# Performance work log

Hardware: AMD Instinct MI355X
Metric: run time of the kernel (lower is better)

Reference implementation:

```python
import jax, jax.numpy as jnp
import numpy as np

N_NODES = 100000
N_EDGES = 1600000
IN_F = 128
HID = 128
OUT_F = 40


def _gcn_conv(x, W, b, src, dst):
    # PyG GCNConv: h = x @ W; out[dst] += norm * h[src]; out += b
    n = x.shape[0]
    h = x @ W  # [N, out_channels]
    deg = jnp.zeros((n,), h.dtype).at[dst].add(jnp.ones((dst.shape[0],), h.dtype))
    dinv = jnp.where(deg > 0, jax.lax.rsqrt(deg), 0.0)  # deg^{-1/2}
    norm = dinv[src] * dinv[dst]  # [E+N]
    msg = h[src] * norm[:, None]  # [E+N, out_channels] gather
    out = jnp.zeros_like(h).at[dst].add(msg)  # scatter-add at targets
    if b is not None:
        out = out + b
    return out


def setup_inputs() -> dict:
    key = jax.random.key(0)
    k_x, k_e, k1, k2, k3, kb1, kb2 = jax.random.split(key, 7)
    x = jax.random.normal(k_x, (N_NODES, IN_F), dtype=jnp.float32)
    edge_index = jax.random.randint(k_e, (2, N_EDGES), 0, N_NODES, dtype=jnp.int64)
    s_in = 1.0 / np.sqrt(IN_F)
    s_h = 1.0 / np.sqrt(HID)
    W_in = jax.random.normal(k1, (IN_F, HID), dtype=jnp.float32) * s_in
    b_in = jnp.zeros((HID,), dtype=jnp.float32)
    W_mid = jax.random.normal(k2, (HID, HID), dtype=jnp.float32) * s_h
    b_mid = jnp.zeros((HID,), dtype=jnp.float32)
    W_out = jax.random.normal(k3, (HID, OUT_F), dtype=jnp.float32) * s_h
    return {"x": x, "edge_index": edge_index, "W_in": W_in, "b_in": b_in,
            "W_mid": W_mid, "b_mid": b_mid, "W_out": W_out}


def reference(x, edge_index, W_in, b_in, W_mid, b_mid, W_out):
    n = x.shape[0]
    loops = jnp.arange(n, dtype=edge_index.dtype)
    src = jnp.concatenate([edge_index[0], loops])  # add self-loops
    dst = jnp.concatenate([edge_index[1], loops])
    h = jax.nn.relu(_gcn_conv(x, W_in, b_in, src, dst))
    h = jax.nn.relu(_gcn_conv(h, W_mid, b_mid, src, dst))
    h = _gcn_conv(h, W_out, None, src, dst)  # out_conv: bias=False
    return jax.nn.log_softmax(h, axis=1)
```

## Files before the change

### kernel.cpp

```cpp
#include <hip/hip_runtime.h>
#include <math.h>

#define N_NODES 100000
#define N_EDGES 1600000
#define NBUCK 391
#define BSTRIDE 4608

typedef __attribute__((ext_vector_type(8))) _Float16 h8v;
typedef __attribute__((ext_vector_type(4))) float f32x4;
typedef __attribute__((ext_vector_type(2))) int i32x2;

#define GEMM_GRID 625
#define NTILES 3125


__global__ void k_prep(const int* __restrict__ srcv, const int* __restrict__ dstv,
                       int* __restrict__ bcnt, unsigned int* __restrict__ ebuf,
                       const float* __restrict__ x, const float* __restrict__ W1,
                       const float* __restrict__ W2, const float* __restrict__ W3,
                       _Float16* __restrict__ Wt,
                       _Float16* __restrict__ bufA, _Float16* __restrict__ bufB,
                       _Float16* __restrict__ zbuf) {
    const int tid = threadIdx.x;
    const int bid = blockIdx.x;

    if (bid < 625) {
        const int lane = tid & 63;
        const int wi = tid >> 6;
        const int nb = wi * 32;
        const int nn = lane & 15;
        const int quad = lane >> 4;
        const int kq = quad * 8;

        h8v bh[4][2], bl[4][2];
#pragma unroll
        for (int c = 0; c < 4; c++)
#pragma unroll
            for (int t = 0; t < 2; t++) {
#pragma unroll
                for (int j = 0; j < 8; j++) {
                    float w = W1[(c * 32 + kq + j) * 128 + nb + t * 16 + nn];
                    _Float16 hi = (_Float16)w;
                    bh[c][t][j] = hi;
                    bl[c][t][j] = (_Float16)(w - (float)hi);
                }
            }

        for (int rt = bid; rt < NTILES; rt += GEMM_GRID) {
            const int r0 = rt * 32;
            f32x4 acc[2][2] = {};
#pragma unroll
            for (int c = 0; c < 4; c++) {
                h8v a[2];
#pragma unroll
                for (int m = 0; m < 2; m++) {
                    const float* p = x + (size_t)(r0 + m * 16 + nn) * 128 + c * 32 + kq;
                    float4 p0 = *(const float4*)p;
                    float4 p1 = *(const float4*)(p + 4);
                    h8v av = {(_Float16)p0.x, (_Float16)p0.y, (_Float16)p0.z, (_Float16)p0.w,
                              (_Float16)p1.x, (_Float16)p1.y, (_Float16)p1.z, (_Float16)p1.w};
                    a[m] = av;
                }
#pragma unroll
                for (int m = 0; m < 2; m++)
#pragma unroll
                    for (int t = 0; t < 2; t++) {
                        acc[m][t] = __builtin_amdgcn_mfma_f32_16x16x32_f16(a[m], bh[c][t], acc[m][t], 0, 0, 0);
                        acc[m][t] = __builtin_amdgcn_mfma_f32_16x16x32_f16(a[m], bl[c][t], acc[m][t], 0, 0, 0);
                    }
            }
#pragma unroll
            for (int m = 0; m < 2; m++)
#pragma unroll
                for (int reg = 0; reg < 4; reg++) {
                    int r = r0 + m * 16 + quad * 4 + reg;
#pragma unroll
                    for (int t = 0; t < 2; t++)
                        bufA[(size_t)r * 128 + nb + t * 16 + nn] = (_Float16)acc[m][t][reg];
                }
        }
        return;
    }

    if (bid >= 1016) {
        if (bid == 1104) {
            if (tid < 128) {
                bufA[(size_t)N_NODES * 128 + tid] = (_Float16)0.f;
                bufB[(size_t)N_NODES * 128 + tid] = (_Float16)0.f;
            }
            if (tid < 64)  zbuf[(size_t)N_NODES * 64 + tid] = (_Float16)0.f;
            return;
        }
        int idx = (bid - 1016) * 256 + tid;
        if (idx >= 176 * 128) return;
        int n = idx / 128, k = idx % 128;
        _Float16 *ph, *pl;
        float v;
        if (n < 128) {
            v = W2[k * 128 + n];
            ph = Wt + 2 * 128 * 128; pl = Wt + 3 * 128 * 128;
        } else {
            int nloc = n - 128;
            v = (nloc < 40) ? W3[k * 40 + nloc] : 0.f;
            ph = Wt + 4 * 128 * 128; pl = Wt + 4 * 128 * 128 + 48 * 128;
            n = nloc;
        }
        _Float16 hi = (_Float16)v;
        _Float16 lo = (_Float16)(v - (float)hi);
        ph[n * 128 + k] = hi;
        pl[n * 128 + k] = lo;
        return;
    }

    __shared__ int hist[NBUCK];
    __shared__ int cur[NBUCK];
    for (int t = tid; t < NBUCK; t += 256) hist[t] = 0;
    __syncthreads();
    const int base = (bid - 625) * 4096;
#pragma unroll
    for (int i = 0; i < 16; i++) {
        int e = base + i * 256 + tid;
        if (e < N_EDGES) atomicAdd(&hist[dstv[e] >> 8], 1);
    }
    __syncthreads();
    for (int t = tid; t < NBUCK; t += 256)
        if (hist[t]) cur[t] = t * BSTRIDE + atomicAdd(&bcnt[t], hist[t]);
    __syncthreads();
#pragma unroll
    for (int i = 0; i < 16; i++) {
        int e = base + i * 256 + tid;
        if (e < N_EDGES) {
            int d = dstv[e];
            int p = atomicAdd(&cur[d >> 8], 1);
            ebuf[p] = ((unsigned int)srcv[e] << 8) | (unsigned int)(d & 255);
        }
    }
}

__launch_bounds__(256)
__global__ void k_bucket(const unsigned int* __restrict__ ebuf, const int* __restrict__ bcnt,
                         i32x2* __restrict__ rowse, float* __restrict__ dinv,
                         int* __restrict__ colidx) {
    __shared__ int cnt[256];
    __shared__ int s[256];
    __shared__ int cur[256];
    const int tid = threadIdx.x;
    const int b = blockIdx.x;
    if (b == 0 && tid == 0) dinv[N_NODES] = 0.f;
    const int e0 = b * BSTRIDE;
    const int e1 = e0 + bcnt[b];
    cnt[tid] = 0;
    __syncthreads();
    for (int e = e0 + tid; e < e1; e += 256) atomicAdd(&cnt[ebuf[e] & 255u], 1);
    __syncthreads();
    int v = cnt[tid];
    int x = v;
    s[tid] = x;
    __syncthreads();
    for (int d = 1; d < 256; d <<= 1) {
        int t = (tid >= d) ? s[tid - d] : 0;
        __syncthreads();
        x += t;
        s[tid] = x;
        __syncthreads();
    }
    int start = e0 + x - v;
    int node = b * 256 + tid;
    if (node < N_NODES) {
        i32x2 se;
        se.x = start;
        se.y = start + v;
        rowse[node] = se;
        dinv[node] = rsqrtf((float)(v + 1));
    }
    cur[tid] = start;
    __syncthreads();
    for (int e = e0 + tid; e < e1; e += 256) {
        unsigned int sd = ebuf[e];
        int pos = atomicAdd(&cur[sd & 255u], 1);
        colidx[pos] = (int)(sd >> 8);
    }
}


__launch_bounds__(256)
__global__ void k_fused128(const _Float16* __restrict__ hp, const i32x2* __restrict__ rowse,
                           const int* __restrict__ colidx, const float* __restrict__ bias,
                           const float* __restrict__ dinv,
                           const _Float16* __restrict__ Wthi, const _Float16* __restrict__ Wtlo,
                           _Float16* __restrict__ out) {
    __shared__ __align__(16) _Float16 As[16 * 128];
    const int lane = threadIdx.x & 63;
    const int wi = threadIdx.x >> 6;
    const int nn = lane & 15;
    const int quad = lane >> 4;
    const int r0 = blockIdx.x * 16;

    {
        const int rl = wi * 4 + quad;
        const int r = r0 + rl;
        const i32x2 se = rowse[r];
        const int deg = se.y - se.x;
        int m = deg;
        m = max(m, __shfl_xor(m, 16));
        m = max(m, __shfl_xor(m, 32));
        const _Float16* hpc = hp + nn * 8;
        float accf[8] = {};
        for (int it = 0; it < m; it += 4) {
            int i0 = se.x + it;
            int s0 = colidx[i0];
            int s1 = colidx[i0 + 1];
            int s2 = colidx[i0 + 2];
            int s3 = colidx[i0 + 3];
            s0 = (it < deg) ? s0 : N_NODES;
            s1 = (it + 1 < deg) ? s1 : N_NODES;
            s2 = (it + 2 < deg) ? s2 : N_NODES;
            s3 = (it + 3 < deg) ? s3 : N_NODES;
            float d0 = dinv[s0];
            float d1 = dinv[s1];
            float d2 = dinv[s2];
            float d3 = dinv[s3];
            h8v v0 = *(const h8v*)(hpc + (size_t)s0 * 128);
            h8v v1 = *(const h8v*)(hpc + (size_t)s1 * 128);
            h8v v2 = *(const h8v*)(hpc + (size_t)s2 * 128);
            h8v v3 = *(const h8v*)(hpc + (size_t)s3 * 128);
#pragma unroll
            for (int j = 0; j < 8; j++) {
                accf[j] = fmaf(d0, (float)v0[j], accf[j]);
                accf[j] = fmaf(d1, (float)v1[j], accf[j]);
                accf[j] = fmaf(d2, (float)v2[j], accf[j]);
                accf[j] = fmaf(d3, (float)v3[j], accf[j]);
            }
        }
        h8v sv = *(const h8v*)(hpc + (size_t)r * 128);
        float dv = rsqrtf((float)(deg + 1));
        const float* bp = bias + nn * 8;
        float4 b0 = *(const float4*)bp;
        float4 b1 = *(const float4*)(bp + 4);
        float bb[8] = {b0.x, b0.y, b0.z, b0.w, b1.x, b1.y, b1.z, b1.w};
        h8v o;
#pragma unroll
        for (int j = 0; j < 8; j++) {
            float sx = accf[j] + dv * (float)sv[j];
            o[j] = (_Float16)fmaxf(fmaf(dv, sx, bb[j]), 0.f);
        }
        *(h8v*)(As + rl * 128 + ((nn ^ rl) * 8)) = o;
    }
    __syncthreads();

    const int nb = wi * 32;
    const int kq = quad * 8;
    f32x4 acc2[2] = {};
#pragma unroll
    for (int c = 0; c < 4; c++) {
        int ch = (c * 4 + quad) ^ nn;
        h8v a = *(const h8v*)(As + nn * 128 + ch * 8);
#pragma unroll
        for (int t = 0; t < 2; t++) {
            int off = (nb + t * 16 + nn) * 128 + c * 32 + kq;
            h8v bhv = *(const h8v*)(Wthi + off);
            h8v blv = *(const h8v*)(Wtlo + off);
            acc2[t] = __builtin_amdgcn_mfma_f32_16x16x32_f16(a, bhv, acc2[t], 0, 0, 0);
            acc2[t] = __builtin_amdgcn_mfma_f32_16x16x32_f16(a, blv, acc2[t], 0, 0, 0);
        }
    }
#pragma unroll
    for (int reg = 0; reg < 4; reg++) {
        int r = r0 + quad * 4 + reg;
#pragma unroll
        for (int t = 0; t < 2; t++)
            out[(size_t)r * 128 + nb + t * 16 + nn] = (_Float16)acc2[t][reg];
    }
}

__launch_bounds__(256)
__global__ void k_fused40(const _Float16* __restrict__ hp, const i32x2* __restrict__ rowse,
                          const int* __restrict__ colidx, const float* __restrict__ bias,
                          const float* __restrict__ dinv,
                          const _Float16* __restrict__ Wthi, const _Float16* __restrict__ Wtlo,
                          _Float16* __restrict__ out) {
    __shared__ __align__(16) _Float16 As[16 * 128];
    const int lane = threadIdx.x & 63;
    const int wi = threadIdx.x >> 6;
    const int nn = lane & 15;
    const int quad = lane >> 4;
    const int r0 = blockIdx.x * 16;

    {
        const int rl = wi * 4 + quad;
        const int r = r0 + rl;
        const i32x2 se = rowse[r];
        const int deg = se.y - se.x;
        int m = deg;
        m = max(m, __shfl_xor(m, 16));
        m = max(m, __shfl_xor(m, 32));
        const _Float16* hpc = hp + nn * 8;
        float accf[8] = {};
        for (int it = 0; it < m; it += 4) {
            int i0 = se.x + it;
            int s0 = colidx[i0];
            int s1 = colidx[i0 + 1];
            int s2 = colidx[i0 + 2];
            int s3 = colidx[i0 + 3];
            s0 = (it < deg) ? s0 : N_NODES;
            s1 = (it + 1 < deg) ? s1 : N_NODES;
            s2 = (it + 2 < deg) ? s2 : N_NODES;
            s3 = (it + 3 < deg) ? s3 : N_NODES;
            float d0 = dinv[s0];
            float d1 = dinv[s1];
            float d2 = dinv[s2];
            float d3 = dinv[s3];
            h8v v0 = *(const h8v*)(hpc + (size_t)s0 * 128);
            h8v v1 = *(const h8v*)(hpc + (size_t)s1 * 128);
            h8v v2 = *(const h8v*)(hpc + (size_t)s2 * 128);
            h8v v3 = *(const h8v*)(hpc + (size_t)s3 * 128);
#pragma unroll
            for (int j = 0; j < 8; j++) {
                accf[j] = fmaf(d0, (float)v0[j], accf[j]);
                accf[j] = fmaf(d1, (float)v1[j], accf[j]);
                accf[j] = fmaf(d2, (float)v2[j], accf[j]);
                accf[j] = fmaf(d3, (float)v3[j], accf[j]);
            }
        }
        h8v sv = *(const h8v*)(hpc + (size_t)r * 128);
        float dv = rsqrtf((float)(deg + 1));
        const float* bp = bias + nn * 8;
        float4 b0 = *(const float4*)bp;
        float4 b1 = *(const float4*)(bp + 4);
        float bb[8] = {b0.x, b0.y, b0.z, b0.w, b1.x, b1.y, b1.z, b1.w};
        h8v o;
#pragma unroll
        for (int j = 0; j < 8; j++) {
            float sx = accf[j] + dv * (float)sv[j];
            o[j] = (_Float16)fmaxf(fmaf(dv, sx, bb[j]), 0.f);
        }
        *(h8v*)(As + rl * 128 + ((nn ^ rl) * 8)) = o;
    }
    __syncthreads();

    if (wi < 3) {
        const int kq = quad * 8;
        f32x4 acc2 = {};
#pragma unroll
        for (int c = 0; c < 4; c++) {
            int ch = (c * 4 + quad) ^ nn;
            h8v a = *(const h8v*)(As + nn * 128 + ch * 8);
            int off = (wi * 16 + nn) * 128 + c * 32 + kq;
            h8v bhv = *(const h8v*)(Wthi + off);
            h8v blv = *(const h8v*)(Wtlo + off);
            acc2 = __builtin_amdgcn_mfma_f32_16x16x32_f16(a, bhv, acc2, 0, 0, 0);
            acc2 = __builtin_amdgcn_mfma_f32_16x16x32_f16(a, blv, acc2, 0, 0, 0);
        }
#pragma unroll
        for (int reg = 0; reg < 4; reg++) {
            int r = r0 + quad * 4 + reg;
            out[(size_t)r * 64 + wi * 16 + nn] = (_Float16)acc2[reg];
        }
    }
}


__launch_bounds__(256)
__global__ void k_agg_out(const _Float16* __restrict__ hp, const i32x2* __restrict__ rowse,
                          const int* __restrict__ colidx, const float* __restrict__ dinv,
                          float* __restrict__ out) {
    const int lane = threadIdx.x & 63;
    const int wid = (blockIdx.x * blockDim.x + threadIdx.x) >> 6;
    const int rs = lane >> 3;
    const int cp = lane & 7;
    const int r = wid * 8 + rs;

    const i32x2 se = rowse[r];
    const int deg = se.y - se.x;
    int m = deg;
    m = max(m, __shfl_xor(m, 8));
    m = max(m, __shfl_xor(m, 16));
    m = max(m, __shfl_xor(m, 32));

    const _Float16* hpc = hp + cp * 8;
    float accf[8] = {};
    for (int it = 0; it < m; it += 4) {
        int i0 = se.x + it;
        int s0 = colidx[i0];
        int s1 = colidx[i0 + 1];
        int s2 = colidx[i0 + 2];
        int s3 = colidx[i0 + 3];
        s0 = (it < deg) ? s0 : N_NODES;
        s1 = (it + 1 < deg) ? s1 : N_NODES;
        s2 = (it + 2 < deg) ? s2 : N_NODES;
        s3 = (it + 3 < deg) ? s3 : N_NODES;
        float d0 = dinv[s0];
        float d1 = dinv[s1];
        float d2 = dinv[s2];
        float d3 = dinv[s3];
        h8v v0 = *(const h8v*)(hpc + (size_t)s0 * 64);
        h8v v1 = *(const h8v*)(hpc + (size_t)s1 * 64);
        h8v v2 = *(const h8v*)(hpc + (size_t)s2 * 64);
        h8v v3 = *(const h8v*)(hpc + (size_t)s3 * 64);
#pragma unroll
        for (int j = 0; j < 8; j++) {
            accf[j] = fmaf(d0, (float)v0[j], accf[j]);
            accf[j] = fmaf(d1, (float)v1[j], accf[j]);
            accf[j] = fmaf(d2, (float)v2[j], accf[j]);
            accf[j] = fmaf(d3, (float)v3[j], accf[j]);
        }
    }

    h8v sv = *(const h8v*)(hpc + (size_t)r * 64);
    float dv = rsqrtf((float)(deg + 1));
    float z[8];
#pragma unroll
    for (int j = 0; j < 8; j++) z[j] = dv * (accf[j] + dv * (float)sv[j]);

    const bool act = cp < 5;
    float pm = -INFINITY;
    if (act) {
#pragma unroll
        for (int j = 0; j < 8; j++) pm = fmaxf(pm, z[j]);
    }
    pm = fmaxf(pm, __shfl_xor(pm, 1));
    pm = fmaxf(pm, __shfl_xor(pm, 2));
    pm = fmaxf(pm, __shfl_xor(pm, 4));
    float pe = 0.f;
    if (act) {
#pragma unroll
        for (int j = 0; j < 8; j++) pe += __expf(z[j] - pm);
    }
    pe += __shfl_xor(pe, 1);
    pe += __shfl_xor(pe, 2);
    pe += __shfl_xor(pe, 4);
    float lse = __logf(pe);
    if (act) {
        float* po = out + (size_t)r * 40 + cp * 8;
        float4 o0 = make_float4(z[0] - pm - lse, z[1] - pm - lse, z[2] - pm - lse, z[3] - pm - lse);
        float4 o1 = make_float4(z[4] - pm - lse, z[5] - pm - lse, z[6] - pm - lse, z[7] - pm - lse);
        *(float4*)po = o0;
        *(float4*)(po + 4) = o1;
    }
}


extern "C" void kernel_launch(void* const* d_in, const int* in_sizes, int n_in,
                              void* d_out, int out_size, void* d_ws, size_t ws_size,
                              hipStream_t stream) {
    const float* x     = (const float*)d_in[0];
    const int*   ei    = (const int*)d_in[1];
    const float* W_in  = (const float*)d_in[2];
    const float* b_in  = (const float*)d_in[3];
    const float* W_mid = (const float*)d_in[4];
    const float* b_mid = (const float*)d_in[5];
    const float* W_out = (const float*)d_in[6];
    float* out = (float*)d_out;

    const int* srcv = ei;
    const int* dstv = ei + N_EDGES;

    char* w = (char*)d_ws;
    float* dinv   = (float*)(w);
    i32x2* rowse  = (i32x2*)(w + (1ull << 19));
    int* bcnt     = (int*)(w + 1507328);
    int* colidx   = (int*)(w + (2ull << 20));
    unsigned int* ebuf = (unsigned int*)(w + (10ull << 20));
    _Float16* Wt  = (_Float16*)(w + (18ull << 20));
    _Float16* bufA = (_Float16*)(w + (19ull << 20));
    _Float16* bufB = (_Float16*)(w + (45ull << 20));
    _Float16* zbuf = (_Float16*)(w + (71ull << 20));

    _Float16* W2h = Wt + 2 * 128 * 128;
    _Float16* W2l = Wt + 3 * 128 * 128;
    _Float16* W3h = Wt + 4 * 128 * 128;
    _Float16* W3l = Wt + 4 * 128 * 128 + 48 * 128;

    (void)hipMemsetAsync(bcnt, 0, NBUCK * sizeof(int), stream);
    k_prep<<<1105, 256, 0, stream>>>(srcv, dstv, bcnt, ebuf, x, W_in, W_mid, W_out,
                                     Wt, bufA, bufB, zbuf);
    k_bucket<<<NBUCK, 256, 0, stream>>>(ebuf, bcnt, rowse, dinv, colidx);

    k_fused128<<<N_NODES / 16, 256, 0, stream>>>(bufA, rowse, colidx, b_in, dinv, W2h, W2l, bufB);
    k_fused40<<<N_NODES / 16, 256, 0, stream>>>(bufB, rowse, colidx, b_mid, dinv, W3h, W3l, zbuf);
    k_agg_out<<<N_NODES / 32, 256, 0, stream>>>(zbuf, rowse, colidx, dinv, out);
}
```

Before: 347.9 us.

## Prescale features by source dinv so aggregation becomes plain fp16 sums

Moves the source-side D^-1/2 normalization out of the gather loops. The first-layer features are prescaled in the bucket kernel, and the GEMM outputs of the later layers are multiplied by dinv[r] before they are stored. The inner aggregation loops then drop the per-edge dinv gathers and the fp32 FMAs, and use packed fp16 vector adds instead. The accumulators are now fp16 rather than fp32, which risks precision loss and overflow. The padding node's zero row now comes from bufA, zbuf or bufB already being zero, since dinv[N_NODES] is no longer written.

```diff
diff --git a/kernel.cpp b/kernel.cpp
--- a/kernel.cpp
+++ b/kernel.cpp
@@ -137,16 +137,17 @@
     }
 }
 
+
 __launch_bounds__(256)
 __global__ void k_bucket(const unsigned int* __restrict__ ebuf, const int* __restrict__ bcnt,
                          i32x2* __restrict__ rowse, float* __restrict__ dinv,
-                         int* __restrict__ colidx) {
+                         int* __restrict__ colidx, _Float16* __restrict__ bufA) {
     __shared__ int cnt[256];
     __shared__ int s[256];
     __shared__ int cur[256];
+    __shared__ float sdv[256];
     const int tid = threadIdx.x;
     const int b = blockIdx.x;
-    if (b == 0 && tid == 0) dinv[N_NODES] = 0.f;
     const int e0 = b * BSTRIDE;
     const int e1 = e0 + bcnt[b];
     cnt[tid] = 0;
@@ -166,12 +167,14 @@
     }
     int start = e0 + x - v;
     int node = b * 256 + tid;
+    float dvv = rsqrtf((float)(v + 1));
+    sdv[tid] = dvv;
     if (node < N_NODES) {
         i32x2 se;
         se.x = start;
         se.y = start + v;
         rowse[node] = se;
-        dinv[node] = rsqrtf((float)(v + 1));
+        dinv[node] = dvv;
     }
     cur[tid] = start;
     __syncthreads();
@@ -179,6 +182,23 @@
         unsigned int sd = ebuf[e];
         int pos = atomicAdd(&cur[sd & 255u], 1);
         colidx[pos] = (int)(sd >> 8);
+    }
+    __syncthreads();
+    const int b0row = b * 256;
+    const int chunk = tid & 15;
+#pragma unroll
+    for (int i = 0; i < 16; i++) {
+        int rl = i * 16 + (tid >> 4);
+        int row = b0row + rl;
+        if (row < N_NODES) {
+            _Float16* p = bufA + (size_t)row * 128 + chunk * 8;
+            h8v vv = *(const h8v*)p;
+            float d = sdv[rl];
+            h8v o;
+#pragma unroll
+            for (int j = 0; j < 8; j++) o[j] = (_Float16)(d * (float)vv[j]);
+            *(h8v*)p = o;
+        }
     }
 }
 
@@ -205,7 +225,7 @@
         m = max(m, __shfl_xor(m, 16));
         m = max(m, __shfl_xor(m, 32));
         const _Float16* hpc = hp + nn * 8;
-        float accf[8] = {};
+        h8v acc = {};
         for (int it = 0; it < m; it += 4) {
             int i0 = se.x + it;
             int s0 = colidx[i0];
@@ -216,21 +236,14 @@
             s1 = (it + 1 < deg) ? s1 : N_NODES;
             s2 = (it + 2 < deg) ? s2 : N_NODES;
             s3 = (it + 3 < deg) ? s3 : N_NODES;
-            float d0 = dinv[s0];
-            float d1 = dinv[s1];
-            float d2 = dinv[s2];
-            float d3 = dinv[s3];
             h8v v0 = *(const h8v*)(hpc + (size_t)s0 * 128);
             h8v v1 = *(const h8v*)(hpc + (size_t)s1 * 128);
             h8v v2 = *(const h8v*)(hpc + (size_t)s2 * 128);
             h8v v3 = *(const h8v*)(hpc + (size_t)s3 * 128);
-#pragma unroll
-            for (int j = 0; j < 8; j++) {
-                accf[j] = fmaf(d0, (float)v0[j], accf[j]);
-                accf[j] = fmaf(d1, (float)v1[j], accf[j]);
-                accf[j] = fmaf(d2, (float)v2[j], accf[j]);
-                accf[j] = fmaf(d3, (float)v3[j], accf[j]);
-            }
+            acc += v0;
+            acc += v1;
+            acc += v2;
+            acc += v3;
         }
         h8v sv = *(const h8v*)(hpc + (size_t)r * 128);
         float dv = rsqrtf((float)(deg + 1));
@@ -241,7 +254,7 @@
         h8v o;
 #pragma unroll
         for (int j = 0; j < 8; j++) {
-            float sx = accf[j] + dv * (float)sv[j];
+            float sx = (float)acc[j] + (float)sv[j];
             o[j] = (_Float16)fmaxf(fmaf(dv, sx, bb[j]), 0.f);
         }
         *(h8v*)(As + rl * 128 + ((nn ^ rl) * 8)) = o;
@@ -267,9 +280,10 @@
 #pragma unroll
     for (int reg = 0; reg < 4; reg++) {
         int r = r0 + quad * 4 + reg;
+        float dr = dinv[r];
 #pragma unroll
         for (int t = 0; t < 2; t++)
-            out[(size_t)r * 128 + nb + t * 16 + nn] = (_Float16)acc2[t][reg];
+            out[(size_t)r * 128 + nb + t * 16 + nn] = (_Float16)(acc2[t][reg] * dr);
     }
 }
 
@@ -295,7 +309,7 @@
         m = max(m, __shfl_xor(m, 16));
         m = max(m, __shfl_xor(m, 32));
         const _Float16* hpc = hp + nn * 8;
-        float accf[8] = {};
+        h8v acc = {};
         for (int it = 0; it < m; it += 4) {
             int i0 = se.x + it;
             int s0 = colidx[i0];
@@ -306,21 +320,14 @@
             s1 = (it + 1 < deg) ? s1 : N_NODES;
             s2 = (it + 2 < deg) ? s2 : N_NODES;
             s3 = (it + 3 < deg) ? s3 : N_NODES;
-            float d0 = dinv[s0];
-            float d1 = dinv[s1];
-            float d2 = dinv[s2];
-            float d3 = dinv[s3];
             h8v v0 = *(const h8v*)(hpc + (size_t)s0 * 128);
             h8v v1 = *(const h8v*)(hpc + (size_t)s1 * 128);
             h8v v2 = *(const h8v*)(hpc + (size_t)s2 * 128);
             h8v v3 = *(const h8v*)(hpc + (size_t)s3 * 128);
-#pragma unroll
-            for (int j = 0; j < 8; j++) {
-                accf[j] = fmaf(d0, (float)v0[j], accf[j]);
-                accf[j] = fmaf(d1, (float)v1[j], accf[j]);
-                accf[j] = fmaf(d2, (float)v2[j], accf[j]);
-                accf[j] = fmaf(d3, (float)v3[j], accf[j]);
-            }
+            acc += v0;
+            acc += v1;
+            acc += v2;
+            acc += v3;
         }
         h8v sv = *(const h8v*)(hpc + (size_t)r * 128);
         float dv = rsqrtf((float)(deg + 1));
@@ -331,7 +338,7 @@
         h8v o;
 #pragma unroll
         for (int j = 0; j < 8; j++) {
-            float sx = accf[j] + dv * (float)sv[j];
+            float sx = (float)acc[j] + (float)sv[j];
             o[j] = (_Float16)fmaxf(fmaf(dv, sx, bb[j]), 0.f);
         }
         *(h8v*)(As + rl * 128 + ((nn ^ rl) * 8)) = o;
@@ -354,7 +361,8 @@
 #pragma unroll
         for (int reg = 0; reg < 4; reg++) {
             int r = r0 + quad * 4 + reg;
-            out[(size_t)r * 64 + wi * 16 + nn] = (_Float16)acc2[reg];
+            float dr = dinv[r];
+            out[(size_t)r * 64 + wi * 16 + nn] = (_Float16)(acc2[reg] * dr);
         }
     }
 }
@@ -362,8 +370,7 @@
 
 __launch_bounds__(256)
 __global__ void k_agg_out(const _Float16* __restrict__ hp, const i32x2* __restrict__ rowse,
-                          const int* __restrict__ colidx, const float* __restrict__ dinv,
-                          float* __restrict__ out) {
+                          const int* __restrict__ colidx, float* __restrict__ out) {
     const int lane = threadIdx.x & 63;
     const int wid = (blockIdx.x * blockDim.x + threadIdx.x) >> 6;
     const int rs = lane >> 3;
@@ -378,7 +385,7 @@
     m = max(m, __shfl_xor(m, 32));
 
     const _Float16* hpc = hp + cp * 8;
-    float accf[8] = {};
+    h8v acc = {};
     for (int it = 0; it < m; it += 4) {
         int i0 = se.x + it;
         int s0 = colidx[i0];
@@ -389,28 +396,21 @@
         s1 = (it + 1 < deg) ? s1 : N_NODES;
         s2 = (it + 2 < deg) ? s2 : N_NODES;
         s3 = (it + 3 < deg) ? s3 : N_NODES;
-        float d0 = dinv[s0];
-        float d1 = dinv[s1];
-        float d2 = dinv[s2];
-        float d3 = dinv[s3];
         h8v v0 = *(const h8v*)(hpc + (size_t)s0 * 64);
         h8v v1 = *(const h8v*)(hpc + (size_t)s1 * 64);
         h8v v2 = *(const h8v*)(hpc + (size_t)s2 * 64);
         h8v v3 = *(const h8v*)(hpc + (size_t)s3 * 64);
-#pragma unroll
-        for (int j = 0; j < 8; j++) {
-            accf[j] = fmaf(d0, (float)v0[j], accf[j]);
-            accf[j] = fmaf(d1, (float)v1[j], accf[j]);
-            accf[j] = fmaf(d2, (float)v2[j], accf[j]);
-            accf[j] = fmaf(d3, (float)v3[j], accf[j]);
-        }
+        acc += v0;
+        acc += v1;
+        acc += v2;
+        acc += v3;
     }
 
     h8v sv = *(const h8v*)(hpc + (size_t)r * 64);
     float dv = rsqrtf((float)(deg + 1));
     float z[8];
 #pragma unroll
-    for (int j = 0; j < 8; j++) z[j] = dv * (accf[j] + dv * (float)sv[j]);
+    for (int j = 0; j < 8; j++) z[j] = dv * ((float)acc[j] + (float)sv[j]);
 
     const bool act = cp < 5;
     float pm = -INFINITY;
@@ -474,9 +474,9 @@
     (void)hipMemsetAsync(bcnt, 0, NBUCK * sizeof(int), stream);
     k_prep<<<1105, 256, 0, stream>>>(srcv, dstv, bcnt, ebuf, x, W_in, W_mid, W_out,
                                      Wt, bufA, bufB, zbuf);
-    k_bucket<<<NBUCK, 256, 0, stream>>>(ebuf, bcnt, rowse, dinv, colidx);
+    k_bucket<<<NBUCK, 256, 0, stream>>>(ebuf, bcnt, rowse, dinv, colidx, bufA);
 
     k_fused128<<<N_NODES / 16, 256, 0, stream>>>(bufA, rowse, colidx, b_in, dinv, W2h, W2l, bufB);
     k_fused40<<<N_NODES / 16, 256, 0, stream>>>(bufB, rowse, colidx, b_mid, dinv, W3h, W3l, zbuf);
-    k_agg_out<<<N_NODES / 32, 256, 0, stream>>>(zbuf, rowse, colidx, dinv, out);
-}
+    k_agg_out<<<N_NODES / 32, 256, 0, stream>>>(zbuf, rowse, colidx, out);
+}
```

Measured after the change: 353.8 us. No clear change (+1.7%).
